# Kernel tuning notes

Measured on AMD Instinct MI355X. Metric: run time of the kernel, lower is better.

## Reference

```python
import jax, jax.numpy as jnp
import numpy as np

NTOKEN = 32000
NWE = 512
NHID_T = 64
NHID_RNN = 1024
NTS = 100
S, B = 128, 32


def setup_inputs() -> dict:
    key = jax.random.key(0)
    ks = jax.random.split(key, 20)
    sc = 0.02
    inp = {}
    inp['text'] = jax.random.randint(ks[0], (S, B), 0, NTOKEN, dtype=jnp.int32)
    inp['timestep'] = jax.random.randint(ks[1], (B,), 0, NTS, dtype=jnp.int32)
    inp['U_weight'] = jax.random.normal(ks[2], (NTOKEN, NWE), jnp.float32) * sc
    inp['trans_W'] = jax.random.normal(ks[3], (NHID_T * NHID_T, NWE), jnp.float32) * sc
    inp['trans_b'] = jnp.zeros((NHID_T * NHID_T,), jnp.float32)
    inp['tc_W1'] = jax.random.normal(ks[4], (NHID_T, 1), jnp.float32) * sc
    inp['tc_b1'] = jnp.zeros((NHID_T,), jnp.float32)
    inp['tc_W2'] = jax.random.normal(ks[5], (NHID_T, NHID_T), jnp.float32) * sc
    inp['tc_b2'] = jnp.zeros((NHID_T,), jnp.float32)
    inp['dw_W'] = jax.random.normal(ks[6], (NWE, NHID_T), jnp.float32) * sc
    inp['dw_b'] = jnp.zeros((NWE,), jnp.float32)
    # 2-layer LSTM, PyTorch gate order (i, f, g, o)
    inp['Wih0'] = jax.random.normal(ks[7], (4 * NHID_RNN, NWE), jnp.float32) * sc
    inp['Whh0'] = jax.random.normal(ks[8], (4 * NHID_RNN, NHID_RNN), jnp.float32) * sc
    inp['bih0'] = jnp.zeros((4 * NHID_RNN,), jnp.float32)
    inp['bhh0'] = jnp.zeros((4 * NHID_RNN,), jnp.float32)
    inp['Wih1'] = jax.random.normal(ks[9], (4 * NHID_RNN, NHID_RNN), jnp.float32) * sc
    inp['Whh1'] = jax.random.normal(ks[10], (4 * NHID_RNN, NHID_RNN), jnp.float32) * sc
    inp['bih1'] = jnp.zeros((4 * NHID_RNN,), jnp.float32)
    inp['bhh1'] = jnp.zeros((4 * NHID_RNN,), jnp.float32)
    inp['dec_W'] = jax.random.normal(ks[11], (NTOKEN, NHID_RNN), jnp.float32) * sc
    inp['dec_b'] = jnp.zeros((NTOKEN,), jnp.float32)
    return inp


def _lstm_layer(x, Wih, Whh, bih, bhh):
    # x: [S, B, Din] -> [S, B, H]
    H = Whh.shape[1]
    Bn = x.shape[1]
    # precompute input projections for all timesteps (one big GEMM)
    xp = jnp.einsum('sbd,gd->sbg', x, Wih) + bih + bhh  # [S, B, 4H]

    def step(carry, xt):
        h, c = carry
        gates = xt + h @ Whh.T  # [B, 4H]
        i, f, g, o = jnp.split(gates, 4, axis=-1)
        i = jax.nn.sigmoid(i)
        f = jax.nn.sigmoid(f)
        g = jnp.tanh(g)
        o = jax.nn.sigmoid(o)
        c = f * c + i * g
        h = o * jnp.tanh(c)
        return (h, c), h

    h0 = jnp.zeros((Bn, H), x.dtype)
    c0 = jnp.zeros((Bn, H), x.dtype)
    _, ys = jax.lax.scan(step, (h0, c0), xp)
    return ys


def reference(text, timestep, U_weight, trans_W, trans_b, tc_W1, tc_b1, tc_W2, tc_b2,
              dw_W, dw_b, Wih0, Whh0, bih0, bhh0, Wih1, Whh1, bih1, bhh1, dec_W, dec_b):
    Ss, Bb = text.shape
    d = NHID_T
    ts = timestep.astype(jnp.float32) / NTS                      # [B]
    text_flat = text.reshape(-1)                                 # [N]
    ts_flat = jnp.broadcast_to(ts[None, :], (Ss, Bb)).reshape(-1)  # [N]
    embs = U_weight[text_flat]                                   # [N, nwe]
    transfo = (embs @ trans_W.T + trans_b).reshape(-1, d, d)     # [N, d, d]
    h1 = jnp.tanh(ts_flat[:, None] @ tc_W1.T + tc_b1)            # [N, d]
    ht = jnp.tanh(h1 @ tc_W2.T + tc_b2)                          # [N, d]
    vec = jnp.einsum('nij,nj->ni', transfo, ht)                  # [N, d]
    emb = (vec @ dw_W.T + dw_b).reshape(Ss, Bb, NWE)             # [S, B, nwe]
    out0 = _lstm_layer(emb, Wih0, Whh0, bih0, bhh0)              # [S, B, H]
    out1 = _lstm_layer(out0, Wih1, Whh1, bih1, bhh1)             # [S, B, H]
    logits = out1 @ dec_W.T + dec_b                              # [S, B, ntoken]
    return logits
```

## Files before the change

### kernel.cpp

```cpp
#include <hip/hip_runtime.h>
#include <hip/hip_bf16.h>
#include <stdint.h>

typedef short bf16x8 __attribute__((ext_vector_type(8)));
typedef float f32x4  __attribute__((ext_vector_type(4)));

#define MFMA16(a, b, c) __builtin_amdgcn_mfma_f32_16x16x32_bf16((a), (b), (c), 0, 0, 0)

__device__ __forceinline__ unsigned short f2bf(float x) {
  union { float f; unsigned int u; } v; v.f = x;
  unsigned int u = v.u;
  unsigned int r = (u + 0x7FFFu + ((u >> 16) & 1u)) >> 16;
  return (unsigned short)r;
}

__device__ __forceinline__ bf16x8 pack8(const float* __restrict__ p) {
  bf16x8 r;
#pragma unroll
  for (int i = 0; i < 8; i++) r[i] = (short)f2bf(p[i]);
  return r;
}

__device__ __forceinline__ bf16x8 ldb8(const unsigned short* __restrict__ p) {
  return *(const bf16x8*)p;
}

__device__ __forceinline__ float sigm(float x) { return 1.0f / (1.0f + expf(-x)); }

__global__ void k_prep(const int* __restrict__ timestep, const float* __restrict__ tc_W1,
                       const float* __restrict__ tc_b1, const float* __restrict__ tc_W2,
                       const float* __restrict__ tc_b2, const float* __restrict__ trans_b,
                       float* __restrict__ ht, float* __restrict__ vbias) {
  __shared__ float h1l[64];
  __shared__ float htl[64];
  int b = blockIdx.x, j = threadIdx.x;
  float ts = (float)timestep[b] / 100.0f;
  h1l[j] = tanhf(ts * tc_W1[j] + tc_b1[j]);
  __syncthreads();
  float s = tc_b2[j];
  for (int m = 0; m < 64; m++) s += tc_W2[j * 64 + m] * h1l[m];
  float h = tanhf(s);
  htl[j] = h;
  ht[b * 64 + j] = h;
  __syncthreads();
  float vb = 0.f;
  for (int m = 0; m < 64; m++) vb += trans_b[j * 64 + m] * htl[m];
  vbias[b * 64 + j] = vb;
}

__global__ void k_M(const float* __restrict__ trans_W, const float* __restrict__ ht,
                    float* __restrict__ M) {
  __shared__ float htl[4][64];
  int i = blockIdx.x;
  int b0 = blockIdx.y * 4;
  int tid = threadIdx.x;
  if (tid < 256) htl[tid >> 6][tid & 63] = ht[(b0 + (tid >> 6)) * 64 + (tid & 63)];
  __syncthreads();
  int k = tid;
  float acc[4] = {0.f, 0.f, 0.f, 0.f};
  for (int j = 0; j < 64; j++) {
    float w = trans_W[(i * 64 + j) * 512 + k];
#pragma unroll
    for (int bb = 0; bb < 4; bb++) acc[bb] += htl[bb][j] * w;
  }
#pragma unroll
  for (int bb = 0; bb < 4; bb++) M[((b0 + bb) * 64 + i) * 512 + k] = acc[bb];
}

__global__ void k_vec(const int* __restrict__ text, const float* __restrict__ U,
                      const float* __restrict__ M, const float* __restrict__ vbias,
                      unsigned short* __restrict__ vec) {
  __shared__ float el[16][512];
  int b = blockIdx.x, sc = blockIdx.y, tid = threadIdx.x;
  for (int idx = tid; idx < 16 * 512; idx += 256) {
    int ss = idx >> 9, k = idx & 511;
    int tok = text[(sc * 16 + ss) * 32 + b];
    el[ss][k] = U[tok * 512 + k];
  }
  __syncthreads();
  int i = tid & 63, sg = tid >> 6;
  float acc[4] = {0.f, 0.f, 0.f, 0.f};
  const float* Mr = M + (b * 64 + i) * 512;
  for (int k = 0; k < 512; k++) {
    float m = Mr[k];
#pragma unroll
    for (int st = 0; st < 4; st++) acc[st] += m * el[sg * 4 + st][k];
  }
  float vb = vbias[b * 64 + i];
#pragma unroll
  for (int st = 0; st < 4; st++) {
    int s = sc * 16 + sg * 4 + st;
    vec[(s * 32 + b) * 64 + i] = f2bf(acc[st] + vb);
  }
}

__global__ void k_A0(const float* __restrict__ Wih0, const float* __restrict__ dw_W,
                     const float* __restrict__ dw_b, const float* __restrict__ bih0,
                     const float* __restrict__ bhh0, float* __restrict__ A0,
                     float* __restrict__ c0) {
  int tid = threadIdx.x;
  int wave = tid >> 6, lane = tid & 63;
  for (int gg = 0; gg < 16; gg++) {
    int g = blockIdx.x * 64 + wave * 16 + gg;
    const float* wr = Wih0 + g * 512;
    float acc = 0.f;
    for (int e = 0; e < 512; e++) acc += wr[e] * dw_W[e * 64 + lane];
    A0[g * 64 + lane] = acc;
    float p = 0.f;
#pragma unroll
    for (int e8 = 0; e8 < 8; e8++) { int e = e8 * 64 + lane; p += wr[e] * dw_b[e]; }
#pragma unroll
    for (int off = 32; off > 0; off >>= 1) p += __shfl_down(p, off);
    if (lane == 0) c0[g] = p + bih0[g] + bhh0[g];
  }
}

__global__ void __launch_bounds__(256, 1)
k_lstm(const unsigned short* __restrict__ vec, const float* __restrict__ A0,
       const float* __restrict__ c0, const float* __restrict__ Whh0,
       const float* __restrict__ Wih1, const float* __restrict__ Whh1,
       const float* __restrict__ bih1, const float* __restrict__ bhh1,
       unsigned short* __restrict__ h0buf, unsigned short* __restrict__ h1buf,
       unsigned short* __restrict__ out0, unsigned short* __restrict__ out1,
       unsigned int* __restrict__ cnt0, unsigned int* __restrict__ cnt1) {
  __shared__ float exch[4][32][64];
  const int tid = threadIdx.x;
  const int wave = tid >> 6, lane = tid & 63;
  const int l15 = lane & 15, quad = lane >> 4;
  const int blk = blockIdx.x;
  const f32x4 fzero = {0.f, 0.f, 0.f, 0.f};

  if (blk < 64) {
    const int colbase = blk * 16;
    bf16x8 bh[4][8];
    bf16x8 bv[4];
#pragma unroll
    for (int nt = 0; nt < 4; nt++) {
      int row = nt * 1024 + colbase + l15;
      const float* wr = Whh0 + row * 1024;
#pragma unroll
      for (int s8 = 0; s8 < 8; s8++) {
        int k = (wave * 8 + s8) * 32 + quad * 8;
        bh[nt][s8] = pack8(wr + k);
      }
      if (wave < 2) bv[nt] = pack8(A0 + row * 64 + wave * 32 + quad * 8);
    }
    float c0v[2][4];
#pragma unroll
    for (int e2 = 0; e2 < 2; e2++) {
      int e = tid + e2 * 256;
      int hcol = e & 15;
#pragma unroll
      for (int g = 0; g < 4; g++) c0v[e2][g] = c0[g * 1024 + colbase + hcol];
    }
    float cst[2] = {0.f, 0.f};

    for (int t = 0; t < 128; t++) {
      if (t > 0) {
        if (tid == 0) {
          while (__hip_atomic_load(&cnt0[t - 1], __ATOMIC_ACQUIRE, __HIP_MEMORY_SCOPE_AGENT) < 64u)
            __builtin_amdgcn_s_sleep(2);
        }
        __syncthreads();
      }
      const unsigned short* hb = h0buf + (t & 1) * 32768;
      f32x4 acc[2][4];
#pragma unroll
      for (int mt = 0; mt < 2; mt++)
#pragma unroll
        for (int nt = 0; nt < 4; nt++) acc[mt][nt] = fzero;

#pragma unroll
      for (int s8 = 0; s8 < 8; s8++) {
        int k = (wave * 8 + s8) * 32 + quad * 8;
        bf16x8 a0 = ldb8(hb + l15 * 1024 + k);
        bf16x8 a1 = ldb8(hb + (16 + l15) * 1024 + k);
#pragma unroll
        for (int nt = 0; nt < 4; nt++) {
          acc[0][nt] = MFMA16(a0, bh[nt][s8], acc[0][nt]);
          acc[1][nt] = MFMA16(a1, bh[nt][s8], acc[1][nt]);
        }
      }
      if (wave < 2) {
        int k = wave * 32 + quad * 8;
        const unsigned short* vp = vec + (t * 32) * 64;
        bf16x8 a0 = ldb8(vp + l15 * 64 + k);
        bf16x8 a1 = ldb8(vp + (16 + l15) * 64 + k);
#pragma unroll
        for (int nt = 0; nt < 4; nt++) {
          acc[0][nt] = MFMA16(a0, bv[nt], acc[0][nt]);
          acc[1][nt] = MFMA16(a1, bv[nt], acc[1][nt]);
        }
      }
#pragma unroll
      for (int mt = 0; mt < 2; mt++)
#pragma unroll
        for (int nt = 0; nt < 4; nt++)
#pragma unroll
          for (int r = 0; r < 4; r++)
            exch[wave][mt * 16 + quad * 4 + r][nt * 16 + l15] = acc[mt][nt][r];
      __syncthreads();

#pragma unroll
      for (int e2 = 0; e2 < 2; e2++) {
        int e = tid + e2 * 256;
        int hcol = e & 15, b = e >> 4;
        float g4[4];
#pragma unroll
        for (int g = 0; g < 4; g++) {
          int col = g * 16 + hcol;
          g4[g] = exch[0][b][col] + exch[1][b][col] + exch[2][b][col] + exch[3][b][col] + c0v[e2][g];
        }
        float ii = sigm(g4[0]), ff = sigm(g4[1]), gg = tanhf(g4[2]), oo = sigm(g4[3]);
        cst[e2] = ff * cst[e2] + ii * gg;
        float h = oo * tanhf(cst[e2]);
        unsigned short hb16 = f2bf(h);
        h0buf[((t + 1) & 1) * 32768 + b * 1024 + colbase + hcol] = hb16;
        out0[(t * 32 + b) * 1024 + colbase + hcol] = hb16;
      }
      __syncthreads();
      if (tid == 0)
        __hip_atomic_fetch_add(&cnt0[t], 1u, __ATOMIC_RELEASE, __HIP_MEMORY_SCOPE_AGENT);
    }
  } else {
    const int blk1 = blk - 64;
    const int colbase = blk1 * 8;
    bf16x8 bfr[2][16];
#pragma unroll
    for (int nt = 0; nt < 2; nt++) {
      int c = nt * 16 + l15;
      int row = (c >> 3) * 1024 + colbase + (c & 7);
#pragma unroll
      for (int ls = 0; ls < 16; ls++) {
        int s = wave * 16 + ls;
        const float* W = (s < 32) ? Wih1 : Whh1;
        int k = ((s < 32) ? s : (s - 32)) * 32 + quad * 8;
        bfr[nt][ls] = pack8(W + row * 1024 + k);
      }
    }
    int hcol = tid & 7, b = tid >> 3;
    float b1v[4];
#pragma unroll
    for (int g = 0; g < 4; g++) {
      int row = g * 1024 + colbase + hcol;
      b1v[g] = bih1[row] + bhh1[row];
    }
    float cst = 0.f;

    for (int t = 0; t < 128; t++) {
      if (tid == 0) {
        while (__hip_atomic_load(&cnt0[t], __ATOMIC_ACQUIRE, __HIP_MEMORY_SCOPE_AGENT) < 64u)
          __builtin_amdgcn_s_sleep(2);
        if (t > 0)
          while (__hip_atomic_load(&cnt1[t - 1], __ATOMIC_ACQUIRE, __HIP_MEMORY_SCOPE_AGENT) < 128u)
            __builtin_amdgcn_s_sleep(2);
      }
      __syncthreads();
      const unsigned short* h1 = h1buf + (t & 1) * 32768;
      const unsigned short* o0 = out0 + (t * 32) * 1024;
      f32x4 acc[2][2];
      acc[0][0] = fzero; acc[0][1] = fzero; acc[1][0] = fzero; acc[1][1] = fzero;
#pragma unroll
      for (int ls = 0; ls < 16; ls++) {
        int s = wave * 16 + ls;
        const unsigned short* A = (s < 32) ? o0 : h1;
        int k = ((s < 32) ? s : (s - 32)) * 32 + quad * 8;
        bf16x8 a0 = ldb8(A + l15 * 1024 + k);
        bf16x8 a1 = ldb8(A + (16 + l15) * 1024 + k);
#pragma unroll
        for (int nt = 0; nt < 2; nt++) {
          acc[0][nt] = MFMA16(a0, bfr[nt][ls], acc[0][nt]);
          acc[1][nt] = MFMA16(a1, bfr[nt][ls], acc[1][nt]);
        }
      }
#pragma unroll
      for (int mt = 0; mt < 2; mt++)
#pragma unroll
        for (int nt = 0; nt < 2; nt++)
#pragma unroll
          for (int r = 0; r < 4; r++)
            exch[wave][mt * 16 + quad * 4 + r][nt * 16 + l15] = acc[mt][nt][r];
      __syncthreads();

      float g4[4];
#pragma unroll
      for (int g = 0; g < 4; g++) {
        int col = g * 8 + hcol;
        g4[g] = exch[0][b][col] + exch[1][b][col] + exch[2][b][col] + exch[3][b][col] + b1v[g];
      }
      float ii = sigm(g4[0]), ff = sigm(g4[1]), gg = tanhf(g4[2]), oo = sigm(g4[3]);
      cst = ff * cst + ii * gg;
      float h = oo * tanhf(cst);
      unsigned short hb16 = f2bf(h);
      h1buf[((t + 1) & 1) * 32768 + b * 1024 + colbase + hcol] = hb16;
      out1[(t * 32 + b) * 1024 + colbase + hcol] = hb16;
      __syncthreads();
      if (tid == 0)
        __hip_atomic_fetch_add(&cnt1[t], 1u, __ATOMIC_RELEASE, __HIP_MEMORY_SCOPE_AGENT);
    }
  }
}

__global__ void __launch_bounds__(256)
k_dec(const unsigned short* __restrict__ out1, const float* __restrict__ dec_W,
      const float* __restrict__ dec_b, float* __restrict__ out) {
  __shared__ unsigned short As[128][72];
  __shared__ unsigned short Bs[128][72];
  const int tid = threadIdx.x;
  const int wave = tid >> 6, lane = tid & 63;
  const int l15 = lane & 15, quad = lane >> 4;
  const int wm = wave & 1, wn = wave >> 1;
  const int mbase = blockIdx.x * 128;
  const int nbase = blockIdx.y * 128;
  const f32x4 fzero = {0.f, 0.f, 0.f, 0.f};
  f32x4 acc[4][4];
#pragma unroll
  for (int a = 0; a < 4; a++)
#pragma unroll
    for (int b = 0; b < 4; b++) acc[a][b] = fzero;

  for (int k0 = 0; k0 < 1024; k0 += 64) {
#pragma unroll
    for (int h = 0; h < 4; h++) {
      int slot = tid + h * 256;
      int r = slot >> 3, c8 = (slot & 7) * 8;
      *(bf16x8*)&As[r][c8] = ldb8(out1 + (mbase + r) * 1024 + k0 + c8);
      *(bf16x8*)&Bs[r][c8] = pack8(dec_W + (nbase + r) * 1024 + k0 + c8);
    }
    __syncthreads();
#pragma unroll
    for (int ks = 0; ks < 2; ks++) {
      bf16x8 af[4], bf[4];
#pragma unroll
      for (int mt = 0; mt < 4; mt++) af[mt] = *(const bf16x8*)&As[wm * 64 + mt * 16 + l15][ks * 32 + quad * 8];
#pragma unroll
      for (int nt = 0; nt < 4; nt++) bf[nt] = *(const bf16x8*)&Bs[wn * 64 + nt * 16 + l15][ks * 32 + quad * 8];
#pragma unroll
      for (int mt = 0; mt < 4; mt++)
#pragma unroll
        for (int nt = 0; nt < 4; nt++) acc[mt][nt] = MFMA16(af[mt], bf[nt], acc[mt][nt]);
    }
    __syncthreads();
  }
#pragma unroll
  for (int mt = 0; mt < 4; mt++)
#pragma unroll
    for (int nt = 0; nt < 4; nt++)
#pragma unroll
      for (int r = 0; r < 4; r++) {
        int row = mbase + wm * 64 + mt * 16 + quad * 4 + r;
        int col = nbase + wn * 64 + nt * 16 + l15;
        out[row * 32000 + col] = acc[mt][nt][r] + dec_b[col];
      }
}

extern "C" void kernel_launch(void* const* d_in, const int* in_sizes, int n_in,
                              void* d_out, int out_size, void* d_ws, size_t ws_size,
                              hipStream_t stream) {
  const int*   text    = (const int*)d_in[0];
  const int*   tstep   = (const int*)d_in[1];
  const float* U       = (const float*)d_in[2];
  const float* trans_W = (const float*)d_in[3];
  const float* trans_b = (const float*)d_in[4];
  const float* tc_W1   = (const float*)d_in[5];
  const float* tc_b1   = (const float*)d_in[6];
  const float* tc_W2   = (const float*)d_in[7];
  const float* tc_b2   = (const float*)d_in[8];
  const float* dw_W    = (const float*)d_in[9];
  const float* dw_b    = (const float*)d_in[10];
  const float* Wih0    = (const float*)d_in[11];
  const float* Whh0    = (const float*)d_in[12];
  const float* bih0    = (const float*)d_in[13];
  const float* bhh0    = (const float*)d_in[14];
  const float* Wih1    = (const float*)d_in[15];
  const float* Whh1    = (const float*)d_in[16];
  const float* bih1    = (const float*)d_in[17];
  const float* bhh1    = (const float*)d_in[18];
  const float* dec_W   = (const float*)d_in[19];
  const float* dec_b   = (const float*)d_in[20];

  char* ws = (char*)d_ws;
  float* ht            = (float*)(ws + 0);
  float* vbias         = (float*)(ws + 8192);
  float* Mbuf          = (float*)(ws + 16384);
  unsigned short* vecb = (unsigned short*)(ws + 4210688);
  float* A0            = (float*)(ws + 4734976);
  float* c0            = (float*)(ws + 5783552);
  unsigned short* h0b  = (unsigned short*)(ws + 5799936);
  unsigned short* h1b  = (unsigned short*)(ws + 5931008);
  unsigned short* o0   = (unsigned short*)(ws + 6062080);
  unsigned short* o1   = (unsigned short*)(ws + 14450688);
  unsigned int* cnt0   = (unsigned int*)(ws + 22839296);
  unsigned int* cnt1   = (unsigned int*)(ws + 22839808);

  (void)hipMemsetAsync(ws + 5799936, 0, 262144, stream);
  (void)hipMemsetAsync(ws + 22839296, 0, 1024, stream);

  k_prep<<<32, 64, 0, stream>>>(tstep, tc_W1, tc_b1, tc_W2, tc_b2, trans_b, ht, vbias);
  k_M<<<dim3(64, 8), 512, 0, stream>>>(trans_W, ht, Mbuf);
  k_vec<<<dim3(32, 8), 256, 0, stream>>>(text, U, Mbuf, vbias, vecb);
  k_A0<<<64, 256, 0, stream>>>(Wih0, dw_W, dw_b, bih0, bhh0, A0, c0);

  k_lstm<<<192, 256, 0, stream>>>(vecb, A0, c0, Whh0, Wih1, Whh1, bih1, bhh1,
                                  h0b, h1b, o0, o1, cnt0, cnt1);

  k_dec<<<dim3(32, 250), 256, 0, stream>>>(o1, dec_W, dec_b, (float*)d_out);
}
```

Baseline: 3.190 ms.

## Replace atomic counters with per-block flags polled by whole waves in LSTM

Cross-block synchronisation in the persistent LSTM kernel changes from one atomic counter per timestep, polled by a single thread with sleeps, to one monotonic flag per block that every wave polls directly with a wave-wide vote. In layer 1, the waves that depend on layer 0 and the waves that depend on the layer-1 recurrence now wait separately. Hidden-state stores are packed into 32-bit agent-scope stores, A-operand loads are batched before the MFMAs, and the LDS exchange buffer is padded to reduce bank conflicts. The spin loops give up after a fixed count, which could let a block read stale state if a producer is slow. The fence-based relaxed store/acquire protocol also has weaker ordering guarantees than the old release/acquire atomics.

```diff
diff --git a/kernel.cpp b/kernel.cpp
--- a/kernel.cpp
+++ b/kernel.cpp
@@ -26,6 +26,13 @@
 }
 
 __device__ __forceinline__ float sigm(float x) { return 1.0f / (1.0f + expf(-x)); }
+
+__device__ __forceinline__ void st_agent(unsigned int* p, unsigned int v) {
+  __hip_atomic_store(p, v, __ATOMIC_RELAXED, __HIP_MEMORY_SCOPE_AGENT);
+}
+__device__ __forceinline__ unsigned int ld_agent(const unsigned int* p) {
+  return __hip_atomic_load(p, __ATOMIC_RELAXED, __HIP_MEMORY_SCOPE_AGENT);
+}
 
 __global__ void k_prep(const int* __restrict__ timestep, const float* __restrict__ tc_W1,
                        const float* __restrict__ tc_b1, const float* __restrict__ tc_W2,
@@ -122,13 +129,14 @@
        const float* __restrict__ bih1, const float* __restrict__ bhh1,
        unsigned short* __restrict__ h0buf, unsigned short* __restrict__ h1buf,
        unsigned short* __restrict__ out0, unsigned short* __restrict__ out1,
-       unsigned int* __restrict__ cnt0, unsigned int* __restrict__ cnt1) {
-  __shared__ float exch[4][32][64];
+       unsigned int* __restrict__ flag0, unsigned int* __restrict__ flag1) {
+  __shared__ float exch[4][32][67];
   const int tid = threadIdx.x;
   const int wave = tid >> 6, lane = tid & 63;
   const int l15 = lane & 15, quad = lane >> 4;
   const int blk = blockIdx.x;
   const f32x4 fzero = {0.f, 0.f, 0.f, 0.f};
+  const unsigned int SPIN_MAX = 1u << 16;
 
   if (blk < 64) {
     const int colbase = blk * 16;
@@ -145,51 +153,56 @@
       }
       if (wave < 2) bv[nt] = pack8(A0 + row * 64 + wave * 32 + quad * 8);
     }
+    const int eb = tid >> 3, ehp = tid & 7;
     float c0v[2][4];
 #pragma unroll
-    for (int e2 = 0; e2 < 2; e2++) {
-      int e = tid + e2 * 256;
-      int hcol = e & 15;
-#pragma unroll
-      for (int g = 0; g < 4; g++) c0v[e2][g] = c0[g * 1024 + colbase + hcol];
-    }
+    for (int p = 0; p < 2; p++)
+#pragma unroll
+      for (int g = 0; g < 4; g++) c0v[p][g] = c0[g * 1024 + colbase + 2 * ehp + p];
     float cst[2] = {0.f, 0.f};
 
     for (int t = 0; t < 128; t++) {
-      if (t > 0) {
-        if (tid == 0) {
-          while (__hip_atomic_load(&cnt0[t - 1], __ATOMIC_ACQUIRE, __HIP_MEMORY_SCOPE_AGENT) < 64u)
-            __builtin_amdgcn_s_sleep(2);
-        }
-        __syncthreads();
-      }
-      const unsigned short* hb = h0buf + (t & 1) * 32768;
-      f32x4 acc[2][4];
-#pragma unroll
-      for (int mt = 0; mt < 2; mt++)
-#pragma unroll
-        for (int nt = 0; nt < 4; nt++) acc[mt][nt] = fzero;
-
-#pragma unroll
-      for (int s8 = 0; s8 < 8; s8++) {
-        int k = (wave * 8 + s8) * 32 + quad * 8;
-        bf16x8 a0 = ldb8(hb + l15 * 1024 + k);
-        bf16x8 a1 = ldb8(hb + (16 + l15) * 1024 + k);
-#pragma unroll
-        for (int nt = 0; nt < 4; nt++) {
-          acc[0][nt] = MFMA16(a0, bh[nt][s8], acc[0][nt]);
-          acc[1][nt] = MFMA16(a1, bh[nt][s8], acc[1][nt]);
-        }
-      }
+      bf16x8 va0, va1;
       if (wave < 2) {
         int k = wave * 32 + quad * 8;
         const unsigned short* vp = vec + (t * 32) * 64;
-        bf16x8 a0 = ldb8(vp + l15 * 64 + k);
-        bf16x8 a1 = ldb8(vp + (16 + l15) * 64 + k);
+        va0 = ldb8(vp + l15 * 64 + k);
+        va1 = ldb8(vp + (16 + l15) * 64 + k);
+      }
+      if (t > 0) {
+        unsigned int tgt = (unsigned int)t, it = 0;
+        while (true) {
+          unsigned int v = ld_agent(&flag0[lane]);
+          if (__all((int)(v >= tgt))) break;
+          if (++it > SPIN_MAX) break;
+        }
+        __builtin_amdgcn_fence(__ATOMIC_ACQUIRE, "agent");
+      }
+      const unsigned short* hb = h0buf + (t & 1) * 32768;
+      bf16x8 ah0[8], ah1[8];
+#pragma unroll
+      for (int s8 = 0; s8 < 8; s8++) {
+        int k = (wave * 8 + s8) * 32 + quad * 8;
+        ah0[s8] = ldb8(hb + l15 * 1024 + k);
+        ah1[s8] = ldb8(hb + (16 + l15) * 1024 + k);
+      }
+      f32x4 acc[2][4];
+#pragma unroll
+      for (int mt = 0; mt < 2; mt++)
+#pragma unroll
+        for (int nt = 0; nt < 4; nt++) acc[mt][nt] = fzero;
+#pragma unroll
+      for (int s8 = 0; s8 < 8; s8++)
 #pragma unroll
         for (int nt = 0; nt < 4; nt++) {
-          acc[0][nt] = MFMA16(a0, bv[nt], acc[0][nt]);
-          acc[1][nt] = MFMA16(a1, bv[nt], acc[1][nt]);
+          acc[0][nt] = MFMA16(ah0[s8], bh[nt][s8], acc[0][nt]);
+          acc[1][nt] = MFMA16(ah1[s8], bh[nt][s8], acc[1][nt]);
+        }
+      if (wave < 2) {
+#pragma unroll
+        for (int nt = 0; nt < 4; nt++) {
+          acc[0][nt] = MFMA16(va0, bv[nt], acc[0][nt]);
+          acc[1][nt] = MFMA16(va1, bv[nt], acc[1][nt]);
         }
       }
 #pragma unroll
@@ -201,26 +214,27 @@
             exch[wave][mt * 16 + quad * 4 + r][nt * 16 + l15] = acc[mt][nt][r];
       __syncthreads();
 
-#pragma unroll
-      for (int e2 = 0; e2 < 2; e2++) {
-        int e = tid + e2 * 256;
-        int hcol = e & 15, b = e >> 4;
+      unsigned short hv[2];
+#pragma unroll
+      for (int p = 0; p < 2; p++) {
+        int hcol = 2 * ehp + p;
         float g4[4];
 #pragma unroll
         for (int g = 0; g < 4; g++) {
           int col = g * 16 + hcol;
-          g4[g] = exch[0][b][col] + exch[1][b][col] + exch[2][b][col] + exch[3][b][col] + c0v[e2][g];
+          g4[g] = exch[0][eb][col] + exch[1][eb][col] + exch[2][eb][col] + exch[3][eb][col] + c0v[p][g];
         }
         float ii = sigm(g4[0]), ff = sigm(g4[1]), gg = tanhf(g4[2]), oo = sigm(g4[3]);
-        cst[e2] = ff * cst[e2] + ii * gg;
-        float h = oo * tanhf(cst[e2]);
-        unsigned short hb16 = f2bf(h);
-        h0buf[((t + 1) & 1) * 32768 + b * 1024 + colbase + hcol] = hb16;
-        out0[(t * 32 + b) * 1024 + colbase + hcol] = hb16;
-      }
+        cst[p] = ff * cst[p] + ii * gg;
+        float h = oo * tanhf(cst[p]);
+        hv[p] = f2bf(h);
+      }
+      unsigned int packed = (unsigned int)hv[0] | ((unsigned int)hv[1] << 16);
+      int off = eb * 1024 + colbase + 2 * ehp;
+      st_agent((unsigned int*)(h0buf + ((t + 1) & 1) * 32768 + off), packed);
+      st_agent((unsigned int*)(out0 + (t * 32) * 1024 + off), packed);
       __syncthreads();
-      if (tid == 0)
-        __hip_atomic_fetch_add(&cnt0[t], 1u, __ATOMIC_RELEASE, __HIP_MEMORY_SCOPE_AGENT);
+      if (tid == 0) st_agent(&flag0[blk], (unsigned int)(t + 1));
     }
   } else {
     const int blk1 = blk - 64;
@@ -238,39 +252,63 @@
         bfr[nt][ls] = pack8(W + row * 1024 + k);
       }
     }
-    int hcol = tid & 7, b = tid >> 3;
-    float b1v[4];
-#pragma unroll
-    for (int g = 0; g < 4; g++) {
-      int row = g * 1024 + colbase + hcol;
-      b1v[g] = bih1[row] + bhh1[row];
-    }
-    float cst = 0.f;
+    const int eb = tid >> 2, ehp = tid & 3;
+    float b1v[2][4];
+    float cst[2] = {0.f, 0.f};
+    if (tid < 128) {
+#pragma unroll
+      for (int p = 0; p < 2; p++)
+#pragma unroll
+        for (int g = 0; g < 4; g++) {
+          int row = g * 1024 + colbase + 2 * ehp + p;
+          b1v[p][g] = bih1[row] + bhh1[row];
+        }
+    }
 
     for (int t = 0; t < 128; t++) {
-      if (tid == 0) {
-        while (__hip_atomic_load(&cnt0[t], __ATOMIC_ACQUIRE, __HIP_MEMORY_SCOPE_AGENT) < 64u)
-          __builtin_amdgcn_s_sleep(2);
-        if (t > 0)
-          while (__hip_atomic_load(&cnt1[t - 1], __ATOMIC_ACQUIRE, __HIP_MEMORY_SCOPE_AGENT) < 128u)
-            __builtin_amdgcn_s_sleep(2);
-      }
-      __syncthreads();
-      const unsigned short* h1 = h1buf + (t & 1) * 32768;
-      const unsigned short* o0 = out0 + (t * 32) * 1024;
+      const unsigned short* Asrc;
+      if (wave < 2) {
+        unsigned int tgt = (unsigned int)(t + 1), it = 0;
+        while (true) {
+          unsigned int v = ld_agent(&flag0[lane]);
+          if (__all((int)(v >= tgt))) break;
+          if (++it > SPIN_MAX) break;
+        }
+        __builtin_amdgcn_fence(__ATOMIC_ACQUIRE, "agent");
+        Asrc = out0 + (t * 32) * 1024;
+      } else {
+        if (t > 0) {
+          unsigned int tgt = (unsigned int)t, it = 0;
+          while (true) {
+            unsigned int v0 = ld_agent(&flag1[lane]);
+            unsigned int v1 = ld_agent(&flag1[64 + lane]);
+            if (__all((int)((v0 >= tgt) & (v1 >= tgt)))) break;
+            if (++it > SPIN_MAX) break;
+          }
+          __builtin_amdgcn_fence(__ATOMIC_ACQUIRE, "agent");
+        }
+        Asrc = h1buf + (t & 1) * 32768;
+      }
       f32x4 acc[2][2];
       acc[0][0] = fzero; acc[0][1] = fzero; acc[1][0] = fzero; acc[1][1] = fzero;
 #pragma unroll
-      for (int ls = 0; ls < 16; ls++) {
-        int s = wave * 16 + ls;
-        const unsigned short* A = (s < 32) ? o0 : h1;
-        int k = ((s < 32) ? s : (s - 32)) * 32 + quad * 8;
-        bf16x8 a0 = ldb8(A + l15 * 1024 + k);
-        bf16x8 a1 = ldb8(A + (16 + l15) * 1024 + k);
-#pragma unroll
-        for (int nt = 0; nt < 2; nt++) {
-          acc[0][nt] = MFMA16(a0, bfr[nt][ls], acc[0][nt]);
-          acc[1][nt] = MFMA16(a1, bfr[nt][ls], acc[1][nt]);
+      for (int hb8 = 0; hb8 < 2; hb8++) {
+        bf16x8 a0[8], a1[8];
+#pragma unroll
+        for (int l8 = 0; l8 < 8; l8++) {
+          int s = wave * 16 + hb8 * 8 + l8;
+          int k = ((s < 32) ? s : (s - 32)) * 32 + quad * 8;
+          a0[l8] = ldb8(Asrc + l15 * 1024 + k);
+          a1[l8] = ldb8(Asrc + (16 + l15) * 1024 + k);
+        }
+#pragma unroll
+        for (int l8 = 0; l8 < 8; l8++) {
+          int ls = hb8 * 8 + l8;
+#pragma unroll
+          for (int nt = 0; nt < 2; nt++) {
+            acc[0][nt] = MFMA16(a0[l8], bfr[nt][ls], acc[0][nt]);
+            acc[1][nt] = MFMA16(a1[l8], bfr[nt][ls], acc[1][nt]);
+          }
         }
       }
 #pragma unroll
@@ -282,21 +320,29 @@
             exch[wave][mt * 16 + quad * 4 + r][nt * 16 + l15] = acc[mt][nt][r];
       __syncthreads();
 
-      float g4[4];
-#pragma unroll
-      for (int g = 0; g < 4; g++) {
-        int col = g * 8 + hcol;
-        g4[g] = exch[0][b][col] + exch[1][b][col] + exch[2][b][col] + exch[3][b][col] + b1v[g];
-      }
-      float ii = sigm(g4[0]), ff = sigm(g4[1]), gg = tanhf(g4[2]), oo = sigm(g4[3]);
-      cst = ff * cst + ii * gg;
-      float h = oo * tanhf(cst);
-      unsigned short hb16 = f2bf(h);
-      h1buf[((t + 1) & 1) * 32768 + b * 1024 + colbase + hcol] = hb16;
-      out1[(t * 32 + b) * 1024 + colbase + hcol] = hb16;
+      if (tid < 128) {
+        unsigned short hv[2];
+#pragma unroll
+        for (int p = 0; p < 2; p++) {
+          int hcol = 2 * ehp + p;
+          float g4[4];
+#pragma unroll
+          for (int g = 0; g < 4; g++) {
+            int col = g * 8 + hcol;
+            g4[g] = exch[0][eb][col] + exch[1][eb][col] + exch[2][eb][col] + exch[3][eb][col] + b1v[p][g];
+          }
+          float ii = sigm(g4[0]), ff = sigm(g4[1]), gg = tanhf(g4[2]), oo = sigm(g4[3]);
+          cst[p] = ff * cst[p] + ii * gg;
+          float h = oo * tanhf(cst[p]);
+          hv[p] = f2bf(h);
+        }
+        unsigned int packed = (unsigned int)hv[0] | ((unsigned int)hv[1] << 16);
+        int off = eb * 1024 + colbase + 2 * ehp;
+        st_agent((unsigned int*)(h1buf + ((t + 1) & 1) * 32768 + off), packed);
+        st_agent((unsigned int*)(out1 + (t * 32) * 1024 + off), packed);
+      }
       __syncthreads();
-      if (tid == 0)
-        __hip_atomic_fetch_add(&cnt1[t], 1u, __ATOMIC_RELEASE, __HIP_MEMORY_SCOPE_AGENT);
+      if (tid == 0) st_agent(&flag1[blk1], (unsigned int)(t + 1));
     }
   }
 }
@@ -390,8 +436,8 @@
   unsigned short* h1b  = (unsigned short*)(ws + 5931008);
   unsigned short* o0   = (unsigned short*)(ws + 6062080);
   unsigned short* o1   = (unsigned short*)(ws + 14450688);
-  unsigned int* cnt0   = (unsigned int*)(ws + 22839296);
-  unsigned int* cnt1   = (unsigned int*)(ws + 22839808);
+  unsigned int* flag0  = (unsigned int*)(ws + 22839296);
+  unsigned int* flag1  = (unsigned int*)(ws + 22839808);
 
   (void)hipMemsetAsync(ws + 5799936, 0, 262144, stream);
   (void)hipMemsetAsync(ws + 22839296, 0, 1024, stream);
@@ -402,7 +448,7 @@
   k_A0<<<64, 256, 0, stream>>>(Wih0, dw_W, dw_b, bih0, bhh0, A0, c0);
 
   k_lstm<<<192, 256, 0, stream>>>(vecb, A0, c0, Whh0, Wih1, Whh1, bih1, bhh1,
-                                  h0b, h1b, o0, o1, cnt0, cnt1);
+                                  h0b, h1b, o0, o1, flag0, flag1);
 
   k_dec<<<dim3(32, 250), 256, 0, stream>>>(o1, dec_W, dec_b, (float*)d_out);
 }
```

Result: faster. 3.098 ms (-2.9%).
